# Kernel optimization log

Hardware: AMD Instinct MI355X
Metric: run time of the kernel (lower is better)

## Reference

```python
import jax, jax.numpy as jnp
import numpy as np

# config: input_shape=(1024,1024), upsampling_scale=4, input_over_output_stride=4
OUT_H = 1024  # int(1024 * 4 / 4)
OUT_W = 1024
SCALE = 4.0 / 4.0  # upscale / stride


def setup_inputs() -> dict:
    key = jax.random.key(0)
    k1, k2 = jax.random.split(key)
    B, N = 128, 256
    # centers anywhere on the grid; wh in [20, 200) so most boxes have nonzero sigma
    boxes_center = jax.random.uniform(k1, (B, N, 2), jnp.float32) * jnp.array([OUT_W, OUT_H], jnp.float32)
    boxes_wh = jax.random.uniform(k2, (B, N, 2), jnp.float32) * 180.0 + 20.0
    return {"boxes_center": boxes_center, "boxes_wh": boxes_wh}


def _forward(boxes_center, boxes_wh):
    Wb = boxes_wh[..., 0]
    Hb = boxes_wh[..., 1]
    # kernel size = W//2*2 - 1 ; radius = (ks-1)//2 ; sigma = radius//3 (all floor-div, as numpy)
    ksw = jnp.floor(Wb / 2) * 2 - 1
    rw = jnp.floor((ksw - 1) / 2)
    sw = jnp.floor(rw / 3)
    ksh = jnp.floor(Hb / 2) * 2 - 1
    rh = jnp.floor((ksh - 1) / 2)
    sh = jnp.floor(rh / 3)

    zero_box = (boxes_center.sum(-1) + boxes_wh.sum(-1)) == 0

    # lmks = (lmks * upscale / stride).astype(int32): truncation toward zero
    x = jnp.trunc(boxes_center[..., 0] * SCALE)
    y = jnp.trunc(boxes_center[..., 1] * SCALE)

    ul0 = x - rw
    ul1 = y - rh
    br0 = x + rw + 1
    br1 = y + rh + 1

    def in_img(a, b):  # is_point_in_img: 0 <= a <= W and 0 <= b <= H (inclusive)
        return (a >= 0) & (a <= OUT_W) & (b >= 0) & (b <= OUT_H)

    active = (~zero_box) & (sw != 0) & (sh != 0) & (in_img(ul0, ul1) | in_img(br0, br1))  # [B,N]

    def splat(center, sig, lo, hi, n):
        # at grid position p, written value = exp(-(p - center)^2 / (2*sigma^2))
        # for p in [max(0, lo), min(n, hi)), since kernel center aligns with `center`.
        p = jnp.arange(n, dtype=jnp.float32)  # [n]
        safe = jnp.where(sig == 0, 1.0, sig)
        g = jnp.exp(-((p - center[..., None]) ** 2) / (2.0 * safe[..., None] ** 2))  # [B,N,n]
        m = (p >= lo[..., None]) & (p < hi[..., None]) & active[..., None]
        return jnp.where(m, g, 0.0)

    vector_x = splat(x, sw, ul0, br0, OUT_W)  # [B,N,OUT_W]
    vector_y = splat(y, sh, ul1, br1, OUT_H)  # [B,N,OUT_H]
    return vector_x, vector_y


def reference(boxes_center, boxes_wh):
    return _forward(boxes_center, boxes_wh)
```

## Files before the change

### kernel.cpp

```cpp
#include <hip/hip_runtime.h>

#define OUT_W 1024
#define OUT_H 1024
#define BOXES_PER_BLOCK 16

typedef float f32x4 __attribute__((ext_vector_type(4)));

__global__ __launch_bounds__(256)
void gv_kernel(const float* __restrict__ center,
               const float* __restrict__ wh,
               float* __restrict__ out_x,
               float* __restrict__ out_y,
               int bn_total)
{
    const int t   = threadIdx.x;
    const int bn0 = blockIdx.x * BOXES_PER_BLOCK;
    const int p0  = t * 4;

#pragma unroll 4
    for (int k = 0; k < BOXES_PER_BLOCK; ++k) {
        const int bn = bn0 + k;
        if (bn >= bn_total) break;

        const float2 c = reinterpret_cast<const float2*>(center)[bn];
        const float2 w = reinterpret_cast<const float2*>(wh)[bn];
        const float cx = c.x, cy = c.y, Wb = w.x, Hb = w.y;

        const float ksw = floorf(Wb * 0.5f) * 2.0f - 1.0f;
        const float rw  = floorf((ksw - 1.0f) * 0.5f);
        const float sw  = floorf(rw / 3.0f);
        const float ksh = floorf(Hb * 0.5f) * 2.0f - 1.0f;
        const float rh  = floorf((ksh - 1.0f) * 0.5f);
        const float sh  = floorf(rh / 3.0f);

        const bool zero_box = ((cx + cy) + (Wb + Hb)) == 0.0f;

        const float x = truncf(cx);
        const float y = truncf(cy);

        const float ul0 = x - rw;
        const float ul1 = y - rh;
        const float br0 = x + rw + 1.0f;
        const float br1 = y + rh + 1.0f;

        const bool in_ul = (ul0 >= 0.0f) && (ul0 <= (float)OUT_W) &&
                           (ul1 >= 0.0f) && (ul1 <= (float)OUT_H);
        const bool in_br = (br0 >= 0.0f) && (br0 <= (float)OUT_W) &&
                           (br1 >= 0.0f) && (br1 <= (float)OUT_H);
        const bool active = (!zero_box) && (sw != 0.0f) && (sh != 0.0f) && (in_ul || in_br);

        const float ssw = (sw == 0.0f) ? 1.0f : sw;
        const float ssh = (sh == 0.0f) ? 1.0f : sh;
        const float iw  = -1.0f / (2.0f * ssw * ssw);
        const float ih  = -1.0f / (2.0f * ssh * ssh);

        f32x4 rx, ry;
#pragma unroll
        for (int i = 0; i < 4; ++i) {
            const float p  = (float)(p0 + i);
            const float dx = p - x;
            const float dy = p - y;
            const bool mx = active && (p >= ul0) && (p < br0);
            const bool my = active && (p >= ul1) && (p < br1);
            rx[i] = mx ? __expf(dx * dx * iw) : 0.0f;
            ry[i] = my ? __expf(dy * dy * ih) : 0.0f;
        }

        const size_t row = (size_t)bn * (OUT_W / 4) + t;
        __builtin_nontemporal_store(rx, reinterpret_cast<f32x4*>(out_x) + row);
        __builtin_nontemporal_store(ry, reinterpret_cast<f32x4*>(out_y) + row);
    }
}

extern "C" void kernel_launch(void* const* d_in, const int* in_sizes, int n_in,
                              void* d_out, int out_size, void* d_ws, size_t ws_size,
                              hipStream_t stream) {
    const float* center = (const float*)d_in[0];
    const float* wh     = (const float*)d_in[1];
    float* out = (float*)d_out;

    const int BN = in_sizes[0] / 2;
    float* out_x = out;
    float* out_y = out + (size_t)BN * OUT_W;

    const int grid = (BN + BOXES_PER_BLOCK - 1) / BOXES_PER_BLOCK;
    gv_kernel<<<dim3(grid), dim3(256), 0, stream>>>(center, wh, out_x, out_y, BN);
}
```

Baseline: 272.5 us.

## Split into bulk zero-fill kernel plus sparse per-box splat kernel

```diff
diff --git a/kernel.cpp b/kernel.cpp
--- a/kernel.cpp
+++ b/kernel.cpp
@@ -2,73 +2,79 @@
 
 #define OUT_W 1024
 #define OUT_H 1024
-#define BOXES_PER_BLOCK 16
 
 typedef float f32x4 __attribute__((ext_vector_type(4)));
 
 __global__ __launch_bounds__(256)
-void gv_kernel(const float* __restrict__ center,
-               const float* __restrict__ wh,
-               float* __restrict__ out_x,
-               float* __restrict__ out_y,
-               int bn_total)
+void zero_kernel(f32x4* __restrict__ out, int n4)
 {
-    const int t   = threadIdx.x;
-    const int bn0 = blockIdx.x * BOXES_PER_BLOCK;
-    const int p0  = t * 4;
+    const int nthreads = gridDim.x * blockDim.x;
+    const f32x4 z = {0.0f, 0.0f, 0.0f, 0.0f};
+    int i = blockIdx.x * blockDim.x + threadIdx.x;
+#pragma unroll 8
+    for (; i < n4; i += nthreads)
+        out[i] = z;
+}
 
-#pragma unroll 4
-    for (int k = 0; k < BOXES_PER_BLOCK; ++k) {
-        const int bn = bn0 + k;
-        if (bn >= bn_total) break;
+__global__ __launch_bounds__(256)
+void splat_kernel(const float* __restrict__ center,
+                  const float* __restrict__ wh,
+                  float* __restrict__ out_x,
+                  float* __restrict__ out_y,
+                  int bn_total)
+{
+    const int lane = threadIdx.x & 63;
+    const int bn   = blockIdx.x * 4 + (threadIdx.x >> 6);
+    if (bn >= bn_total) return;
 
-        const float2 c = reinterpret_cast<const float2*>(center)[bn];
-        const float2 w = reinterpret_cast<const float2*>(wh)[bn];
-        const float cx = c.x, cy = c.y, Wb = w.x, Hb = w.y;
+    const float2 c = reinterpret_cast<const float2*>(center)[bn];
+    const float2 w = reinterpret_cast<const float2*>(wh)[bn];
+    const float cx = c.x, cy = c.y, Wb = w.x, Hb = w.y;
 
-        const float ksw = floorf(Wb * 0.5f) * 2.0f - 1.0f;
-        const float rw  = floorf((ksw - 1.0f) * 0.5f);
-        const float sw  = floorf(rw / 3.0f);
-        const float ksh = floorf(Hb * 0.5f) * 2.0f - 1.0f;
-        const float rh  = floorf((ksh - 1.0f) * 0.5f);
-        const float sh  = floorf(rh / 3.0f);
+    const float ksw = floorf(Wb * 0.5f) * 2.0f - 1.0f;
+    const float rw  = floorf((ksw - 1.0f) * 0.5f);
+    const float sw  = floorf(rw / 3.0f);
+    const float ksh = floorf(Hb * 0.5f) * 2.0f - 1.0f;
+    const float rh  = floorf((ksh - 1.0f) * 0.5f);
+    const float sh  = floorf(rh / 3.0f);
 
-        const bool zero_box = ((cx + cy) + (Wb + Hb)) == 0.0f;
+    const bool zero_box = ((cx + cy) + (Wb + Hb)) == 0.0f;
 
-        const float x = truncf(cx);
-        const float y = truncf(cy);
+    const float x = truncf(cx);
+    const float y = truncf(cy);
 
-        const float ul0 = x - rw;
-        const float ul1 = y - rh;
-        const float br0 = x + rw + 1.0f;
-        const float br1 = y + rh + 1.0f;
+    const float ul0 = x - rw;
+    const float ul1 = y - rh;
+    const float br0 = x + rw + 1.0f;
+    const float br1 = y + rh + 1.0f;
 
-        const bool in_ul = (ul0 >= 0.0f) && (ul0 <= (float)OUT_W) &&
-                           (ul1 >= 0.0f) && (ul1 <= (float)OUT_H);
-        const bool in_br = (br0 >= 0.0f) && (br0 <= (float)OUT_W) &&
-                           (br1 >= 0.0f) && (br1 <= (float)OUT_H);
-        const bool active = (!zero_box) && (sw != 0.0f) && (sh != 0.0f) && (in_ul || in_br);
+    const bool in_ul = (ul0 >= 0.0f) && (ul0 <= (float)OUT_W) &&
+                       (ul1 >= 0.0f) && (ul1 <= (float)OUT_H);
+    const bool in_br = (br0 >= 0.0f) && (br0 <= (float)OUT_W) &&
+                       (br1 >= 0.0f) && (br1 <= (float)OUT_H);
+    const bool active = (!zero_box) && (sw != 0.0f) && (sh != 0.0f) && (in_ul || in_br);
+    if (!active) return;
 
-        const float ssw = (sw == 0.0f) ? 1.0f : sw;
-        const float ssh = (sh == 0.0f) ? 1.0f : sh;
-        const float iw  = -1.0f / (2.0f * ssw * ssw);
-        const float ih  = -1.0f / (2.0f * ssh * ssh);
+    const float iw = -1.0f / (2.0f * sw * sw);
+    const float ih = -1.0f / (2.0f * sh * sh);
 
-        f32x4 rx, ry;
-#pragma unroll
-        for (int i = 0; i < 4; ++i) {
-            const float p  = (float)(p0 + i);
-            const float dx = p - x;
-            const float dy = p - y;
-            const bool mx = active && (p >= ul0) && (p < br0);
-            const bool my = active && (p >= ul1) && (p < br1);
-            rx[i] = mx ? __expf(dx * dx * iw) : 0.0f;
-            ry[i] = my ? __expf(dy * dy * ih) : 0.0f;
+    {
+        float* row = out_x + (size_t)bn * OUT_W;
+        const int lo = max(0, (int)ul0);
+        const int hi = min(OUT_W, (int)br0);
+        for (int p = lo + lane; p < hi; p += 64) {
+            const float d = (float)p - x;
+            row[p] = __expf(d * d * iw);
         }
-
-        const size_t row = (size_t)bn * (OUT_W / 4) + t;
-        __builtin_nontemporal_store(rx, reinterpret_cast<f32x4*>(out_x) + row);
-        __builtin_nontemporal_store(ry, reinterpret_cast<f32x4*>(out_y) + row);
+    }
+    {
+        float* row = out_y + (size_t)bn * OUT_H;
+        const int lo = max(0, (int)ul1);
+        const int hi = min(OUT_H, (int)br1);
+        for (int p = lo + lane; p < hi; p += 64) {
+            const float d = (float)p - y;
+            row[p] = __expf(d * d * ih);
+        }
     }
 }
 
@@ -83,6 +89,9 @@
     float* out_x = out;
     float* out_y = out + (size_t)BN * OUT_W;
 
-    const int grid = (BN + BOXES_PER_BLOCK - 1) / BOXES_PER_BLOCK;
-    gv_kernel<<<dim3(grid), dim3(256), 0, stream>>>(center, wh, out_x, out_y, BN);
+    const int n4 = out_size / 4;
+    zero_kernel<<<dim3(2048), dim3(256), 0, stream>>>((f32x4*)out, n4);
+
+    const int grid = (BN + 3) / 4;
+    splat_kernel<<<dim3(grid), dim3(256), 0, stream>>>(center, wh, out_x, out_y, BN);
 }
```

Result: no change. 276.6 us (+1.5%).
